# Kernel optimization log

Measured on AMD Instinct MI355X. Metric: run time of the kernel, lower is better.

Reference implementation:

```python
import jax, jax.numpy as jnp
import numpy as np

# Multi-scale feature pyramid (H, W) per level: strides 8/16/32/64 on a ~512px image
SHAPES = ((64, 64), (32, 32), (16, 16), (8, 8))
N_HEADS, N_LEVELS, N_POINTS = 8, 4, 4
D_MODEL = 256
HEAD_DIM = D_MODEL // N_HEADS


def setup_inputs() -> dict:
    key = jax.random.key(0)
    ks = jax.random.split(key, 11)
    B, C = 4, D_MODEL
    Lv = sum(h * w for h, w in SHAPES)  # 5440
    Lq = Lv  # encoder self-attention: queries are the flattened features
    scale = 0.02
    return {
        "query": jax.random.normal(ks[0], (B, Lq, C), jnp.float32),
        "reference_points": jax.random.uniform(ks[1], (B, Lq, N_LEVELS, 2), jnp.float32),
        "value": jax.random.normal(ks[2], (B, Lv, C), jnp.float32),
        "W_off": jax.random.normal(ks[3], (C, N_HEADS * N_LEVELS * N_POINTS * 2), jnp.float32) * scale,
        "b_off": jax.random.normal(ks[4], (N_HEADS * N_LEVELS * N_POINTS * 2,), jnp.float32) * 0.5,
        "W_attn": jax.random.normal(ks[5], (C, N_HEADS * N_LEVELS * N_POINTS), jnp.float32) * scale,
        "b_attn": jax.random.normal(ks[6], (N_HEADS * N_LEVELS * N_POINTS,), jnp.float32) * scale,
        "W_val": jax.random.normal(ks[7], (C, C), jnp.float32) * scale,
        "b_val": jax.random.normal(ks[8], (C,), jnp.float32) * scale,
        "W_out": jax.random.normal(ks[9], (C, C), jnp.float32) * scale,
        "b_out": jax.random.normal(ks[10], (C,), jnp.float32) * scale,
    }


def _bilinear_sample(val, grid, H, W):
    """Replicates F.grid_sample(mode='bilinear', padding_mode='zeros', align_corners=False).

    val:  [N, C, H, W]
    grid: [N, Lq, P, 2] in [-1, 1] (x, y order)
    returns: [N, C, Lq, P]
    """
    N, C = val.shape[0], val.shape[1]
    # unnormalize (align_corners=False)
    x = (grid[..., 0] + 1.0) * 0.5 * W - 0.5  # [N, Lq, P]
    y = (grid[..., 1] + 1.0) * 0.5 * H - 0.5
    x0 = jnp.floor(x)
    y0 = jnp.floor(y)
    wx = x - x0  # fractional parts
    wy = y - y0
    flat = val.reshape(N, C, H * W)

    def gather(xi, yi):
        valid = (xi >= 0) & (xi < W) & (yi >= 0) & (yi < H)
        xc = jnp.clip(xi, 0, W - 1).astype(jnp.int32)
        yc = jnp.clip(yi, 0, H - 1).astype(jnp.int32)
        idx = yc * W + xc  # [N, Lq, P]
        g = jax.vmap(lambda v, i: v[:, i])(flat, idx)  # [N, C, Lq, P]
        return g * valid[:, None, :, :].astype(val.dtype)

    out = (gather(x0, y0) * ((1 - wx) * (1 - wy))[:, None]
           + gather(x0 + 1, y0) * (wx * (1 - wy))[:, None]
           + gather(x0, y0 + 1) * ((1 - wx) * wy)[:, None]
           + gather(x0 + 1, y0 + 1) * (wx * wy)[:, None])
    return out


def _ms_deform_attn(query, reference_points, value, W_off, b_off, W_attn, b_attn,
                    W_val, b_val, W_out, b_out):
    B, Lq, C = query.shape
    val = value @ W_val + b_val  # [B, Lv, C]
    val = val.reshape(B, -1, N_HEADS, HEAD_DIM)

    offsets = (query @ W_off + b_off).reshape(B, Lq, N_HEADS, N_LEVELS, N_POINTS, 2)
    weights = jax.nn.softmax(
        (query @ W_attn + b_attn).reshape(B, Lq, N_HEADS, N_LEVELS * N_POINTS), axis=-1
    ).reshape(B, Lq, N_HEADS, N_LEVELS, N_POINTS)

    # offset normalizer: (W, H) per level
    offset_norm = jnp.array([[w, h] for h, w in SHAPES], jnp.float32)
    # ref_dim == 2 branch
    locs = reference_points[:, :, None, :, None, :] + offsets / offset_norm[None, None, None, :, None, :]
    grids = 2.0 * locs - 1.0  # [B, Lq, nh, nl, np, 2]

    acc = jnp.zeros((B * N_HEADS, HEAD_DIM, Lq), query.dtype)
    start = 0
    for lid, (H, W) in enumerate(SHAPES):
        # [B, HW, nh, hd] -> [B*nh, hd, H, W]
        v = val[:, start:start + H * W].transpose(0, 2, 3, 1).reshape(B * N_HEADS, HEAD_DIM, H, W)
        g = grids[:, :, :, lid].transpose(0, 2, 1, 3, 4).reshape(B * N_HEADS, Lq, N_POINTS, 2)
        s = _bilinear_sample(v, g, H, W)  # [B*nh, hd, Lq, np]
        w = weights[:, :, :, lid].transpose(0, 2, 1, 3).reshape(B * N_HEADS, 1, Lq, N_POINTS)
        acc = acc + (s * w).sum(-1)
        start += H * W

    out = acc.reshape(B, D_MODEL, Lq).transpose(0, 2, 1)  # [B, Lq, C]
    return out @ W_out + b_out


def reference(query, reference_points, value, W_off, b_off, W_attn, b_attn,
              W_val, b_val, W_out, b_out):
    return _ms_deform_attn(query, reference_points, value, W_off, b_off,
                           W_attn, b_attn, W_val, b_val, W_out, b_out)
```

## Files before the change

kernel.cpp:

```cpp
#include <hip/hip_runtime.h>


typedef __attribute__((ext_vector_type(8))) _Float16 half8;
typedef __attribute__((ext_vector_type(4))) _Float16 half4;
typedef __attribute__((ext_vector_type(4))) float f32x4;

typedef __attribute__((address_space(3))) unsigned int lds_uint;
typedef const __attribute__((address_space(1))) unsigned int g_uint;

__device__ __forceinline__ void load_lds16(const _Float16* g, _Float16* l) {
    __builtin_amdgcn_global_load_lds((g_uint*)g, (lds_uint*)l, 16, 0, 0);
}

__device__ __forceinline__ half8 splat8(_Float16 v) {
    half8 r = {v, v, v, v, v, v, v, v};
    return r;
}

#define M_TOTAL 21760

__global__ __launch_bounds__(256) void prep_w(
    const float* __restrict__ W_val, const float* __restrict__ W_off,
    const float* __restrict__ W_attn, const float* __restrict__ W_out,
    _Float16* __restrict__ wtf, _Float16* __restrict__ wto)
{
    if (blockIdx.x >= 80) {
        const int s = (blockIdx.x - 80) * 256 + threadIdx.x;
        const int cg = s >> 9;
        const int kt = (s >> 6) & 7;
        const int l = s & 63;
        const int col = cg * 16 + (l & 15);
        const int k0 = kt * 32 + (l >> 4) * 8;
        half8 h;
#pragma unroll
        for (int e = 0; e < 8; ++e)
            h[e] = (_Float16)W_out[(k0 + e) * 256 + col];
        *(half8*)(wto + ((size_t)s << 3)) = h;
        return;
    }
    const int slot = blockIdx.x * 256 + threadIdx.x;
    const int T = slot >> 11;
    const int rem = slot & 2047;
    const int n = rem >> 5;
    const int k0 = (rem & 31) * 8;
    half8 h;
#pragma unroll
    for (int e = 0; e < 8; ++e) {
        const int k = k0 + e;
        float v;
        if (T < 4) {
            v = W_val[k * 256 + T * 64 + n];
        } else {
            const int n2 = (T - 4) * 64 + n;
            v = (n2 < 256) ? W_off[k * 256 + n2] : W_attn[k * 128 + (n2 - 256)];
        }
        h[e] = (_Float16)v;
    }
    const int dbyte = T * 32768 + n * 512 + ((k0 * 2) ^ ((n & 7) << 4));
    *(half8*)(wtf + (dbyte >> 1)) = h;
}

__global__ __launch_bounds__(256) void gemm12_cvt(
    const float* __restrict__ value, const float* __restrict__ query,
    const _Float16* __restrict__ wtf,
    const float* __restrict__ b_val, const float* __restrict__ b_off,
    const float* __restrict__ b_attn,
    _Float16* __restrict__ valh, _Float16* __restrict__ offh)
{
    __shared__ _Float16 Asw[64 * 256];
    __shared__ _Float16 Bsw[64 * 256];

    const int bid = ((int)blockIdx.x % 8) * 425 + ((int)blockIdx.x / 8);

    const bool g1 = bid < 1360;
    const int id = g1 ? bid : bid - 1360;
    const int mt = g1 ? (id >> 2) : (id / 6);
    const int nt = g1 ? (id & 3) : (id % 6);
    const int NN = g1 ? 256 : 384;
    const float* A = g1 ? value : query;
    _Float16* C = g1 ? valh : offh;
    const int bm = mt * 64;
    const int bn = nt * 64;
    const int T  = g1 ? nt : 4 + nt;

    const int tid = threadIdx.x;
    const int wave = tid >> 6, lane = tid & 63;
    const int ml = lane & 15, q = lane >> 4;

    const _Float16* wsrc = wtf + ((size_t)T << 14);
#pragma unroll
    for (int i = 0; i < 8; ++i)
        load_lds16(wsrc + (((size_t)i * 256 + tid) << 3),
                   Bsw + (((size_t)i * 256 + wave * 64) << 3));

    const int rbase = wave * 16;
    float4 pa[16];
#pragma unroll
    for (int rr = 0; rr < 16; ++rr)
        pa[rr] = *(const float4*)(A + (size_t)(bm + rbase + rr) * 256 + lane * 4);
#pragma unroll
    for (int rr = 0; rr < 16; ++rr) {
        const int row = rbase + rr;
        const float4 v = pa[rr];
        const half4 h = {(_Float16)v.x, (_Float16)v.y, (_Float16)v.z, (_Float16)v.w};
        const int wbyte = row * 512 + ((lane * 8) ^ ((row & 7) << 4));
        *(half4*)(Asw + (wbyte >> 1)) = h;
    }

    __syncthreads();

    const int swl = (ml & 7) << 4;
    const int abase = (rbase + ml) * 512;

    const f32x4 zero4 = {0.f, 0.f, 0.f, 0.f};
    f32x4 acc[4] = {zero4, zero4, zero4, zero4};

#pragma unroll
    for (int kt = 0; kt < 8; ++kt) {
        const int koff = (kt * 64 + q * 16) ^ swl;
        const half8 af = *(const half8*)(Asw + ((abase + koff) >> 1));
#pragma unroll
        for (int j = 0; j < 4; ++j) {
            const half8 bf = *(const half8*)(Bsw + ((((j * 16 + ml) * 512) + koff) >> 1));
            acc[j] = __builtin_amdgcn_mfma_f32_16x16x32_f16(af, bf, acc[j], 0, 0, 0);
        }
    }

    const int r0 = q * 4;
#pragma unroll
    for (int j = 0; j < 4; ++j) {
        const int col = bn + j * 16 + ml;
        const float bj = g1 ? b_val[col] : (col < 256 ? b_off[col] : b_attn[col - 256]);
        const size_t rbaseC = (size_t)(bm + rbase + r0) * NN + col;
#pragma unroll
        for (int r = 0; r < 4; ++r)
            C[rbaseC + (size_t)r * NN] = (_Float16)(acc[j][r] + bj);
    }
}

__global__ __launch_bounds__(512) void sample_out(
    const _Float16* __restrict__ valh,
    const float* __restrict__ refp,
    const _Float16* __restrict__ offh,
    const _Float16* __restrict__ wto,
    const float* __restrict__ b_out,
    float* __restrict__ out)
{
    __shared__ _Float16 accT[16 * 256];

    const int bi = (int)blockIdx.x;
    const int xcd = bi & 7, rr_ = bi >> 3;
    const int L = (xcd >> 1) * 340 + (xcd & 1) * 170 + rr_;

    const int tid = threadIdx.x;
    const int wave = tid >> 6, lane = tid & 63;
    const int q2 = lane >> 5, sl = lane & 31;
    const int bql = wave * 2 + q2;
    const int bq = L * 16 + bql;
    const int b = bq / 5440;
    const int h = sl >> 2;
    const int t = sl & 3;
    const int d8 = t * 8;

    const int Wt = 64 >> t;
    const float fW = (float)Wt;

    const half8 ofr = *(const half8*)(offh + (size_t)bq * 384 + h * 32 + t * 8);
    const half4 lgt = *(const half4*)(offh + (size_t)bq * 384 + 256 + h * 16 + t * 4);
    const float2 rxy = *(const float2*)(refp + (size_t)bq * 8 + t * 2);

    float lg[4];
#pragma unroll
    for (int p = 0; p < 4; ++p) lg[p] = (float)lgt[p];

    float mx = fmaxf(fmaxf(lg[0], lg[1]), fmaxf(lg[2], lg[3]));
    mx = fmaxf(mx, __shfl_xor(mx, 1));
    mx = fmaxf(mx, __shfl_xor(mx, 2));
    float s = 0.f;
#pragma unroll
    for (int p = 0; p < 4; ++p) { lg[p] = __expf(lg[p] - mx); s += lg[p]; }
    s += __shfl_xor(s, 1);
    s += __shfl_xor(s, 2);
    const float inv = 1.f / s;

    unsigned pk[16];
#pragma unroll
    for (int p = 0; p < 4; ++p) {
        const float aw = lg[p] * inv;
        const float ox = (float)ofr[p * 2];
        const float oy = (float)ofr[p * 2 + 1];
        const float x = fmaf(rxy.x, fW, ox) - 0.5f;
        const float y = fmaf(rxy.y, fW, oy) - 0.5f;
        const float x0f = floorf(x), y0f = floorf(y);
        const int x0 = (int)x0f, y0 = (int)y0f;
        const float wx = x - x0f, wy = y - y0f;
        const bool okx0 = ((unsigned)x0 < (unsigned)Wt);
        const bool okx1 = ((unsigned)(x0 + 1) < (unsigned)Wt);
        const bool oky0 = ((unsigned)y0 < (unsigned)Wt);
        const bool oky1 = ((unsigned)(y0 + 1) < (unsigned)Wt);
        const int xc0 = min(max(x0, 0), Wt - 1);
        const int xc1 = min(max(x0 + 1, 0), Wt - 1);
        const int yc0 = min(max(y0, 0), Wt - 1);
        const int yc1 = min(max(y0 + 1, 0), Wt - 1);
        const _Float16 w0 = (_Float16)((okx0 & oky0) ? (1.f - wx) * (1.f - wy) * aw : 0.f);
        const _Float16 w1 = (_Float16)((okx1 & oky0) ? wx * (1.f - wy) * aw : 0.f);
        const _Float16 w2 = (_Float16)((okx0 & oky1) ? (1.f - wx) * wy * aw : 0.f);
        const _Float16 w3 = (_Float16)((okx1 & oky1) ? wx * wy * aw : 0.f);
        pk[p * 4 + 0] = ((unsigned)(yc0 * Wt + xc0) << 16) |
                        (unsigned)__builtin_bit_cast(unsigned short, w0);
        pk[p * 4 + 1] = ((unsigned)(yc0 * Wt + xc1) << 16) |
                        (unsigned)__builtin_bit_cast(unsigned short, w1);
        pk[p * 4 + 2] = ((unsigned)(yc1 * Wt + xc0) << 16) |
                        (unsigned)__builtin_bit_cast(unsigned short, w2);
        pk[p * 4 + 3] = ((unsigned)(yc1 * Wt + xc1) << 16) |
                        (unsigned)__builtin_bit_cast(unsigned short, w3);
    }

    const int gbase = lane & ~3;
    const _Float16* vb = valh + ((size_t)(b * 5440)) * 256 + h * 32 + d8;
    const _Float16* v0 = vb;
    const _Float16* v1 = vb + (size_t)4096 * 256;
    const _Float16* v2 = vb + (size_t)5120 * 256;
    const _Float16* v3 = vb + (size_t)5376 * 256;

    unsigned qA[16], qB[16];
    half8 cA[16], cB[16];
    half8 acc = splat8((_Float16)0.f);

#define SHUF(dst, srclane)                                                     \
    {                                                                          \
        _Pragma("unroll") for (int c = 0; c < 16; ++c)                         \
            dst[c] = (unsigned)__shfl((int)pk[c], (srclane));                  \
    }
#define ISSUE(dst, qv, vbase)                                                  \
    __builtin_amdgcn_sched_barrier(0);                                         \
    {                                                                          \
        _Pragma("unroll") for (int c = 0; c < 16; ++c)                         \
            dst[c] = *(const half8*)((vbase) + ((size_t)(qv[c] >> 16) << 8));  \
    }                                                                          \
    __builtin_amdgcn_sched_barrier(0);
#define CONSUME(cv, qv)                                                        \
    {                                                                          \
        _Pragma("unroll") for (int c = 0; c < 16; ++c)                         \
            acc += cv[c] * splat8(__builtin_bit_cast(                          \
                _Float16, (unsigned short)(qv[c] & 0xffffu)));                 \
    }

    SHUF(qA, gbase + 0);
    ISSUE(cA, qA, v0);
    SHUF(qB, gbase + 1);
    ISSUE(cB, qB, v1);
    CONSUME(cA, qA);
    SHUF(qA, gbase + 2);
    ISSUE(cA, qA, v2);
    CONSUME(cB, qB);
    SHUF(qB, gbase + 3);
    ISSUE(cB, qB, v3);
    CONSUME(cA, qA);
    CONSUME(cB, qB);

#undef SHUF
#undef ISSUE
#undef CONSUME

    {
        const int cbyte = (h * 32 + d8) * 2;
        const int wbyte = bql * 512 + (cbyte ^ ((bql & 7) << 4));
        *(half8*)(accT + (wbyte >> 1)) = acc;
    }
    __syncthreads();

    const int ml = lane & 15, q = lane >> 4;
    const int wc0 = wave * 32;
    const f32x4 zero4 = {0.f, 0.f, 0.f, 0.f};
    f32x4 o[2] = {zero4, zero4};

#pragma unroll
    for (int kt = 0; kt < 8; ++kt) {
        const int koff = kt * 64 + q * 16;
        const half8 af = *(const half8*)(accT +
            ((ml * 512 + (koff ^ ((ml & 7) << 4))) >> 1));
#pragma unroll
        for (int j = 0; j < 2; ++j) {
            const half8 bf = *(const half8*)(wto +
                ((((size_t)(wave * 2 + j) * 8 + kt) * 64 + lane) << 3));
            o[j] = __builtin_amdgcn_mfma_f32_16x16x32_f16(af, bf, o[j], 0, 0, 0);
        }
    }

    const int r0 = q * 4;
    const size_t bq0 = (size_t)L * 16;
#pragma unroll
    for (int j = 0; j < 2; ++j) {
        const int col = wc0 + j * 16 + ml;
        const float bj = b_out[col];
#pragma unroll
        for (int r = 0; r < 4; ++r)
            out[(bq0 + r0 + r) * 256 + col] = o[j][r] + bj;
    }
}

extern "C" void kernel_launch(void* const* d_in, const int* in_sizes, int n_in,
                              void* d_out, int out_size, void* d_ws, size_t ws_size,
                              hipStream_t stream) {
    const float* query  = (const float*)d_in[0];
    const float* refp   = (const float*)d_in[1];
    const float* value  = (const float*)d_in[2];
    const float* W_off  = (const float*)d_in[3];
    const float* b_off  = (const float*)d_in[4];
    const float* W_attn = (const float*)d_in[5];
    const float* b_attn = (const float*)d_in[6];
    const float* W_val  = (const float*)d_in[7];
    const float* b_val  = (const float*)d_in[8];
    const float* W_out  = (const float*)d_in[9];
    const float* b_out  = (const float*)d_in[10];
    float* out = (float*)d_out;

    const size_t M = M_TOTAL;

    _Float16* valh  = (_Float16*)d_ws;
    _Float16* offh  = valh + M * 256;
    _Float16* wto   = offh + M * 384;
    _Float16* wtf   = wto + 256 * 256;

    dim3 blk(256);
    prep_w<<<dim3(112), blk, 0, stream>>>(W_val, W_off, W_attn, W_out, wtf, wto);
    gemm12_cvt<<<dim3(3400), blk, 0, stream>>>(
        value, query, wtf, b_val, b_off, b_attn, valh, offh);
    sample_out<<<dim3(M / 16), dim3(512), 0, stream>>>(
        valh, refp, offh, wto, b_out, out);
}
```

Before: 178.0 us.

## Fuse weight prep into GEMM kernel, converting weight tiles directly from fp32

Removes the separate prep_w launch. Each GEMM block now loads its 64-column weight tile straight from the fp32 weights, converts it to fp16 and writes it swizzled into LDS, replacing the async global-to-LDS copy of a pre-converted buffer. The W_out conversion moves into 32 extra blocks of the same launch. This saves one kernel launch and a global round trip, but every one of the 3400 GEMM blocks now re-reads and re-converts fp32 weights with strided scalar loads.

```diff
diff --git a/kernel.cpp b/kernel.cpp
--- a/kernel.cpp
+++ b/kernel.cpp
@@ -7,10 +7,6 @@
 
 typedef __attribute__((address_space(3))) unsigned int lds_uint;
 typedef const __attribute__((address_space(1))) unsigned int g_uint;
-
-__device__ __forceinline__ void load_lds16(const _Float16* g, _Float16* l) {
-    __builtin_amdgcn_global_load_lds((g_uint*)g, (lds_uint*)l, 16, 0, 0);
-}
 
 __device__ __forceinline__ half8 splat8(_Float16 v) {
     half8 r = {v, v, v, v, v, v, v, v};
@@ -19,13 +15,22 @@
 
 #define M_TOTAL 21760
 
-__global__ __launch_bounds__(256) void prep_w(
+__global__ __launch_bounds__(256) void gemm12_cvt(
+    const float* __restrict__ value, const float* __restrict__ query,
     const float* __restrict__ W_val, const float* __restrict__ W_off,
     const float* __restrict__ W_attn, const float* __restrict__ W_out,
-    _Float16* __restrict__ wtf, _Float16* __restrict__ wto)
+    const float* __restrict__ b_val, const float* __restrict__ b_off,
+    const float* __restrict__ b_attn,
+    _Float16* __restrict__ valh, _Float16* __restrict__ offh,
+    _Float16* __restrict__ wto)
 {
-    if (blockIdx.x >= 80) {
-        const int s = (blockIdx.x - 80) * 256 + threadIdx.x;
+    __shared__ _Float16 Asw[64 * 256];
+    __shared__ _Float16 Bsw[64 * 256];
+
+    const int tid = threadIdx.x;
+
+    if (blockIdx.x >= 3400) {
+        const int s = ((int)blockIdx.x - 3400) * 256 + tid;
         const int cg = s >> 9;
         const int kt = (s >> 6) & 7;
         const int l = s & 63;
@@ -38,37 +43,6 @@
         *(half8*)(wto + ((size_t)s << 3)) = h;
         return;
     }
-    const int slot = blockIdx.x * 256 + threadIdx.x;
-    const int T = slot >> 11;
-    const int rem = slot & 2047;
-    const int n = rem >> 5;
-    const int k0 = (rem & 31) * 8;
-    half8 h;
-#pragma unroll
-    for (int e = 0; e < 8; ++e) {
-        const int k = k0 + e;
-        float v;
-        if (T < 4) {
-            v = W_val[k * 256 + T * 64 + n];
-        } else {
-            const int n2 = (T - 4) * 64 + n;
-            v = (n2 < 256) ? W_off[k * 256 + n2] : W_attn[k * 128 + (n2 - 256)];
-        }
-        h[e] = (_Float16)v;
-    }
-    const int dbyte = T * 32768 + n * 512 + ((k0 * 2) ^ ((n & 7) << 4));
-    *(half8*)(wtf + (dbyte >> 1)) = h;
-}
-
-__global__ __launch_bounds__(256) void gemm12_cvt(
-    const float* __restrict__ value, const float* __restrict__ query,
-    const _Float16* __restrict__ wtf,
-    const float* __restrict__ b_val, const float* __restrict__ b_off,
-    const float* __restrict__ b_attn,
-    _Float16* __restrict__ valh, _Float16* __restrict__ offh)
-{
-    __shared__ _Float16 Asw[64 * 256];
-    __shared__ _Float16 Bsw[64 * 256];
 
     const int bid = ((int)blockIdx.x % 8) * 425 + ((int)blockIdx.x / 8);
 
@@ -81,17 +55,34 @@
     _Float16* C = g1 ? valh : offh;
     const int bm = mt * 64;
     const int bn = nt * 64;
-    const int T  = g1 ? nt : 4 + nt;
-
-    const int tid = threadIdx.x;
+
+    const float* W;
+    int sW, nb;
+    if (g1)            { W = W_val;  sW = 256; nb = bn; }
+    else if (nt < 4)   { W = W_off;  sW = 256; nb = bn; }
+    else               { W = W_attn; sW = 128; nb = bn - 256; }
+
     const int wave = tid >> 6, lane = tid & 63;
     const int ml = lane & 15, q = lane >> 4;
 
-    const _Float16* wsrc = wtf + ((size_t)T << 14);
-#pragma unroll
-    for (int i = 0; i < 8; ++i)
-        load_lds16(wsrc + (((size_t)i * 256 + tid) << 3),
-                   Bsw + (((size_t)i * 256 + wave * 64) << 3));
+    {
+        const int bcol = tid & 63;
+        const int bkg = tid >> 6;
+        const float* wS = W + (size_t)(bkg * 64) * sW + nb + bcol;
+        _Float16* bdst = Bsw + ((size_t)bcol * 512 >> 1);
+        const int bswl = (bcol & 7) << 4;
+#pragma unroll
+        for (int u = 0; u < 8; ++u) {
+            float pv[8];
+#pragma unroll
+            for (int e = 0; e < 8; ++e)
+                pv[e] = wS[(size_t)(u * 8 + e) * sW];
+            const half8 hb = {(_Float16)pv[0], (_Float16)pv[1], (_Float16)pv[2], (_Float16)pv[3],
+                              (_Float16)pv[4], (_Float16)pv[5], (_Float16)pv[6], (_Float16)pv[7]};
+            const int kb = (bkg * 64 + u * 8) * 2;
+            *(half8*)(bdst + ((kb ^ bswl) >> 1)) = hb;
+        }
+    }
 
     const int rbase = wave * 16;
     float4 pa[16];
@@ -321,12 +312,11 @@
     _Float16* valh  = (_Float16*)d_ws;
     _Float16* offh  = valh + M * 256;
     _Float16* wto   = offh + M * 384;
-    _Float16* wtf   = wto + 256 * 256;
 
     dim3 blk(256);
-    prep_w<<<dim3(112), blk, 0, stream>>>(W_val, W_off, W_attn, W_out, wtf, wto);
-    gemm12_cvt<<<dim3(3400), blk, 0, stream>>>(
-        value, query, wtf, b_val, b_off, b_attn, valh, offh);
+    gemm12_cvt<<<dim3(3432), blk, 0, stream>>>(
+        value, query, W_val, W_off, W_attn, W_out,
+        b_val, b_off, b_attn, valh, offh, wto);
     sample_out<<<dim3(M / 16), dim3(512), 0, stream>>>(
         valh, refp, offh, wto, b_out, out);
 }
```

Measured after the change: 179.0 us. Within noise of the previous version (+0.5%).
